# Kernel optimization log

Measured on AMD Instinct MI355X. Metric: run time of the kernel, lower is better.

The kernel has to match this reference:

```python
import jax, jax.numpy as jnp
import numpy as np

N_EDGES = 6000
NUM_IMGS = 5  # 1 reference + 4 source views
H = W = 800
NUM_HALF_V = 10  # hardcoded in sample_points_2d


def setup_inputs() -> dict:
    rng = np.random.default_rng(0)
    # 3D edge endpoints in camera space, in front of the camera
    start = rng.normal(0.0, 0.3, (N_EDGES, 3)).astype(np.float32)
    start[:, 2] += 2.5
    d = rng.normal(size=(N_EDGES, 3))
    d /= np.linalg.norm(d, axis=1, keepdims=True)
    length = rng.uniform(0.3, 0.7, (N_EDGES, 1))
    end = (start + d * length).astype(np.float32)
    # num_horizontal = clamp(norm/0.01, 2, 1000) -- integer, no gradient, so
    # the ragged coordinate template is precomputed here (faithful to torch)
    num_h = np.clip((np.linalg.norm(end - start, axis=-1) / 0.01).astype(np.int64), 2, 1000)
    edge_idx_x = np.repeat(np.arange(N_EDGES), num_h)
    begin = np.concatenate(([0], np.cumsum(num_h)[:-1]))
    dx = (np.arange(num_h.sum()) - begin[edge_idx_x]) / (num_h - 1)[edge_idx_x]
    dy = np.arange(NUM_HALF_V) / (NUM_HALF_V - 1)
    dy = np.concatenate((-dy[::-1], dy))  # [20]
    coords_x = np.repeat(dx, 2 * NUM_HALF_V).astype(np.float32)  # [T]
    coords_y = np.tile(dy, int(num_h.sum())).astype(np.float32)  # [T]
    edge_idx = np.repeat(edge_idx_x, 2 * NUM_HALF_V).astype(np.int64)  # [T]
    num_per_edge = (num_h * NUM_HALF_V * 2).astype(np.int64)  # [N]
    imgs = rng.random((NUM_IMGS, H, W)).astype(np.float32)
    intrinsic = np.array([[0.8, 0.0, 0.5], [0.0, 0.8, 0.5], [0.0, 0.0, 1.0]], dtype=np.float32)
    trans = np.zeros((NUM_IMGS - 1, 3, 4), dtype=np.float32)
    for i in range(NUM_IMGS - 1):
        Rt = np.eye(3, 4, dtype=np.float32)
        Rt[:, 3] = rng.normal(0.0, 0.05, 3)
        trans[i] = intrinsic @ Rt
    return {
        'start_points': jnp.asarray(start),
        'end_points': jnp.asarray(end),
        'imgs': jnp.asarray(imgs),
        'transformations': jnp.asarray(trans),
        'intrinsic': jnp.asarray(intrinsic),
        'coords_x': jnp.asarray(coords_x),
        'coords_y': jnp.asarray(coords_y),
        'edge_idx': jnp.asarray(edge_idx),
        'num_per_edge': jnp.asarray(num_per_edge),
    }


def _bilinear(img, uv):
    # img [H,W], uv [T,2] in [0,1); grid_sample(align_corners=False) convention
    Hh, Ww = img.shape
    x = uv[:, 0] * Ww - 0.5
    y = uv[:, 1] * Hh - 0.5
    x0 = jnp.floor(x)
    y0 = jnp.floor(y)
    wx = x - x0
    wy = y - y0
    x0i = jnp.clip(x0.astype(jnp.int32), 0, Ww - 1)
    x1i = jnp.clip(x0i + 1, 0, Ww - 1)
    y0i = jnp.clip(y0.astype(jnp.int32), 0, Hh - 1)
    y1i = jnp.clip(y0i + 1, 0, Hh - 1)
    v00 = img[y0i, x0i]
    v01 = img[y0i, x1i]
    v10 = img[y1i, x0i]
    v11 = img[y1i, x1i]
    return (v00 * (1 - wx) + v01 * wx) * (1 - wy) + (v10 * (1 - wx) + v11 * wx) * wy


def reference(start_points, end_points, imgs, transformations, intrinsic,
              coords_x, coords_y, edge_idx, num_per_edge):
    num_src = imgs.shape[0] - 1
    img_w = imgs.shape[2]
    n_edges = start_points.shape[0]
    # interleave endpoints: [2N,3]
    points_c = jnp.stack([start_points, end_points], axis=1).reshape(-1, 3)

    def sample_template(ep):
        # ep: [N,2,2] projected 2D edge endpoints -> per-coordinate 2D points [T,2]
        p0 = ep[:, 0]
        cur_dir = ep[:, 1] - ep[:, 0]
        dir3 = jnp.concatenate([cur_dir, jnp.zeros_like(cur_dir[:, :1])], axis=1)
        z = jnp.zeros_like(dir3).at[:, 2].set(1.0)
        c = jnp.cross(dir3, z)[:, :2]
        edge_up = c / (jnp.linalg.norm(c, axis=-1, keepdims=True) + 1e-6) * (10.0 / img_w)
        return (cur_dir[edge_idx] * coords_x[:, None]
                + edge_up[edge_idx] * coords_y[:, None]
                + p0[edge_idx])

    # reference view projection (pinhole, normalized coords)
    proj = (intrinsic @ points_c.T).T
    ep1 = (proj[:, :2] / (proj[:, 2:3] + 1e-6)).reshape(-1, 2, 2)
    p2d1 = sample_template(ep1)  # [T,2]
    vm1 = jnp.all((p2d1 > 0) & (p2d1 < 1), axis=-1)
    p2d1 = jnp.clip(p2d1, 0.0, 0.999999)

    # source view projections
    hom = jnp.concatenate([points_c, jnp.ones_like(points_c[:, :1])], axis=1)  # [2N,4]
    projs = jnp.einsum('sij,nj->sni', transformations, hom)
    ep2 = (projs[..., :2] / (projs[..., 2:3] + 1e-6)).reshape(num_src, -1, 2, 2)
    p2d2 = jax.vmap(sample_template)(ep2)  # [S,T,2]
    vm2 = jnp.all((p2d2 > 0) & (p2d2 < 1), axis=-1)
    p2d2 = jnp.clip(p2d2, 0.0, 0.999999)

    # bilinear image sampling (irregular gather)
    s1 = _bilinear(imgs[0], p2d1)  # [T]
    s2 = jax.vmap(_bilinear)(imgs[1:], p2d2)  # [S,T]

    # loss4: per-edge mean squared photometric difference; black-area detection
    cnt = num_per_edge.astype(jnp.float32)
    seg_sum = lambda v: jax.ops.segment_sum(v, edge_idx, num_segments=n_edges)
    diff2 = (s2 - s1[None, :]) ** 2  # [S,T]
    similarity_loss = jax.vmap(seg_sum)(diff2) / cnt[None, :]  # [S,N]
    black_area = (seg_sum((s1 < 0.01).astype(jnp.float32)) / cnt) > 0.5  # [N]

    # scatter_min of per-point validity -> per-edge mask
    sim_mask_pts = (vm1[None, :] & vm2).astype(jnp.int32)  # [S,T]
    seg_min = lambda m: jax.ops.segment_min(m, edge_idx, num_segments=n_edges)
    similarity_mask = jax.vmap(seg_min)(sim_mask_pts).astype(bool)  # [S,N]

    return similarity_loss, similarity_mask, black_area, p2d1, p2d2
```

## Files before the change

### kernel.cpp

```cpp
#include <hip/hip_runtime.h>
#include <math.h>

#define IMG_W   800
#define IMG_PIX (IMG_W * IMG_W)
#define NEDGE   6000
#define NSRC    4
#define NVIEW   5
#define HDR (2 * NSRC * NEDGE + NEDGE)

typedef float vf4 __attribute__((ext_vector_type(4)));
typedef float vf2 __attribute__((ext_vector_type(2)));

struct __attribute__((packed, aligned(4))) f2u { float a, b; };

__device__ __forceinline__ f2u ld2(const float* __restrict__ p) {
    return *(const f2u*)p;
}
__device__ __forceinline__ void nts2(float* p, float a, float b) {
    vf2 v; v.x = a; v.y = b;
    __builtin_nontemporal_store(v, (vf2*)p);
}
__device__ __forceinline__ void nts4(float* p, float a, float b, float c, float d) {
    vf4 v; v.x = a; v.y = b; v.z = c; v.w = d;
    __builtin_nontemporal_store(v, (vf4*)p);
}

__global__ void edge_params(const float* __restrict__ sp,
                            const float* __restrict__ epnt,
                            const float* __restrict__ K,
                            const float* __restrict__ T,
                            float4* __restrict__ prm) {
    int e = blockIdx.x * blockDim.x + threadIdx.x;
    if (e >= NEDGE) return;
    float sx = sp[3 * e], sy = sp[3 * e + 1], sz = sp[3 * e + 2];
    float ex = epnt[3 * e], ey = epnt[3 * e + 1], ez = epnt[3 * e + 2];
    for (int v = 0; v < NVIEW; ++v) {
        float as, bs, cs, ae, be, ce;
        if (v == 0) {
            as = K[0] * sx + K[1] * sy + K[2] * sz;
            bs = K[3] * sx + K[4] * sy + K[5] * sz;
            cs = K[6] * sx + K[7] * sy + K[8] * sz;
            ae = K[0] * ex + K[1] * ey + K[2] * ez;
            be = K[3] * ex + K[4] * ey + K[5] * ez;
            ce = K[6] * ex + K[7] * ey + K[8] * ez;
        } else {
            const float* t = T + (v - 1) * 12;
            as = t[0] * sx + t[1] * sy + t[2] * sz + t[3];
            bs = t[4] * sx + t[5] * sy + t[6] * sz + t[7];
            cs = t[8] * sx + t[9] * sy + t[10] * sz + t[11];
            ae = t[0] * ex + t[1] * ey + t[2] * ez + t[3];
            be = t[4] * ex + t[5] * ey + t[6] * ez + t[7];
            ce = t[8] * ex + t[9] * ey + t[10] * ez + t[11];
        }
        float u0 = as / (cs + 1e-6f);
        float w0 = bs / (cs + 1e-6f);
        float u1 = ae / (ce + 1e-6f);
        float w1 = be / (ce + 1e-6f);
        float dx = u1 - u0, dy = w1 - w0;
        float cxx = dy, cyy = -dx;
        float nrm = sqrtf(cxx * cxx + cyy * cyy);
        float inv = 1.f / (nrm + 1e-6f) * (10.0f / (float)IMG_W);
        prm[(e * NVIEW + v) * 2 + 0] = make_float4(u0, w0, dx, dy);
        prm[(e * NVIEW + v) * 2 + 1] = make_float4(cxx * inv, cyy * inv, 0.f, 0.f);
    }
}

__global__ void __launch_bounds__(256)
scan_kernel(const int* __restrict__ npe, int* __restrict__ bg) {
    __shared__ int part[256];
    int t = threadIdx.x;
    int base = t * 24;
    int loc[24];
    int s = 0;
#pragma unroll
    for (int i = 0; i < 24; ++i) {
        int idx = base + i;
        int v = (idx < NEDGE) ? npe[idx] : 0;
        loc[i] = s;
        s += v;
    }
    part[t] = s;
    __syncthreads();
    int own = s;
    for (int off = 1; off < 256; off <<= 1) {
        int v = (t >= off) ? part[t - off] : 0;
        __syncthreads();
        part[t] += v;
        __syncthreads();
    }
    int myoff = part[t] - own;
#pragma unroll
    for (int i = 0; i < 24; ++i) {
        int idx = base + i;
        if (idx < NEDGE) bg[idx] = myoff + loc[i];
    }
}

__global__ void __launch_bounds__(256)
points_kernel(const int* __restrict__ npe,
              const int* __restrict__ bg,
              const float* __restrict__ imgs,
              const float4* __restrict__ prm,
              float* __restrict__ out,
              int P) {
    const int e = blockIdx.x;
    const int nsamp = npe[e];
    const int nh = nsamp / 20;
    const int b20 = bg[e];

    __shared__ float DX[1000];
    __shared__ float DY[20];
    __shared__ float rS[4][5];
    __shared__ int   rM[4];

    for (int h = threadIdx.x; h < nh; h += 256)
        DX[h] = (float)((double)h / (double)(nh - 1));
    if (threadIdx.x < 20) {
        int m = threadIdx.x;
        DY[m] = (m < 10) ? -(float)((double)(9 - m) / 9.0)
                         :  (float)((double)(m - 10) / 9.0);
    }

    float4 A[NVIEW], B[NVIEW];
    {
        const float4* pe = prm + (size_t)e * (NVIEW * 2);
#pragma unroll
        for (int v = 0; v < NVIEW; ++v) { A[v] = pe[2 * v]; B[v] = pe[2 * v + 1]; }
    }
    __syncthreads();

    float accs[NSRC] = {0.f, 0.f, 0.f, 0.f};
    float accB = 0.f;
    unsigned maskAcc = 0x1Fu;

    for (int base = 0; base < nsamp; base += 256 * 4) {
        const int t = threadIdx.x;
        bool fullIter = (base + 1024) <= nsamp;
        if (fullIter) {
            int pidx[4];
            pidx[0] = base + 2 * t;
            pidx[1] = pidx[0] + 1;
            pidx[2] = pidx[0] + 512;
            pidx[3] = pidx[2] + 1;

            float px[4 * NVIEW], py[4 * NVIEW];
            unsigned vmb[4];
#pragma unroll
            for (int k = 0; k < 4; ++k) {
                int p = pidx[k];
                int h = p / 20;
                int m = p - h * 20;
                float xk = DX[h];
                float yk = DY[m];
                unsigned mb = 0;
#pragma unroll
                for (int v = 0; v < NVIEW; ++v) {
                    float ux = A[v].z * xk + B[v].x * yk + A[v].x;
                    float uy = A[v].w * xk + B[v].y * yk + A[v].y;
                    if ((ux > 0.f) && (ux < 1.f) && (uy > 0.f) && (uy < 1.f)) mb |= (1u << v);
                    px[k * NVIEW + v] = fminf(fmaxf(ux, 0.f), 0.999999f);
                    py[k * NVIEW + v] = fminf(fmaxf(uy, 0.f), 0.999999f);
                }
                vmb[k] = mb;
                maskAcc &= mb;
            }

            size_t gb = (size_t)(b20 + base);
#pragma unroll
            for (int v = 0; v < NVIEW; ++v) {
                float* bp = (v == 0) ? (out + HDR + 2 * gb)
                                     : (out + HDR + 2 * (size_t)P
                                            + 2 * ((size_t)(v - 1) * P + gb));
                nts4(bp + 4 * t,        px[0 * NVIEW + v], py[0 * NVIEW + v],
                                        px[1 * NVIEW + v], py[1 * NVIEW + v]);
                nts4(bp + 1024 + 4 * t, px[2 * NVIEW + v], py[2 * NVIEW + v],
                                        px[3 * NVIEW + v], py[3 * NVIEW + v]);
            }

            f2u r0[4 * NVIEW], r1[4 * NVIEW];
            unsigned hib[4] = {0, 0, 0, 0};
#pragma unroll
            for (int k = 0; k < 4; ++k) {
#pragma unroll
                for (int v = 0; v < NVIEW; ++v) {
                    int j = k * NVIEW + v;
                    float fx = px[j] * (float)IMG_W - 0.5f;
                    float fy = py[j] * (float)IMG_W - 0.5f;
                    float xf = floorf(fx), yf = floorf(fy);
                    px[j] = fx - xf;
                    py[j] = fy - yf;
                    int x0 = (int)xf;
                    int y0 = (int)yf;
                    int xc = min(max(x0, 0), IMG_W - 2);
                    int y0i = min(max(y0, 0), IMG_W - 1);
                    int y1i = min(y0i + 1, IMG_W - 1);
                    if (x0 >= IMG_W - 1) hib[k] |= (1u << v);
                    const float* im = imgs + v * IMG_PIX;
                    r0[j] = ld2(im + y0i * IMG_W + xc);
                    r1[j] = ld2(im + y1i * IMG_W + xc);
                }
            }
#pragma unroll
            for (int k = 0; k < 4; ++k) {
                float sval[NVIEW];
#pragma unroll
                for (int v = 0; v < NVIEW; ++v) {
                    int j = k * NVIEW + v;
                    bool hi = (hib[k] >> v) & 1u;
                    float v00 = hi ? r0[j].b : r0[j].a;
                    float v01 = r0[j].b;
                    float v10 = hi ? r1[j].b : r1[j].a;
                    float v11 = r1[j].b;
                    float wxv = px[j], wyv = py[j];
                    sval[v] = (v00 * (1.f - wxv) + v01 * wxv) * (1.f - wyv)
                            + (v10 * (1.f - wxv) + v11 * wxv) * wyv;
                }
                float s1 = sval[0];
                accB += (s1 < 0.01f) ? 1.f : 0.f;
#pragma unroll
                for (int s = 0; s < NSRC; ++s) {
                    float d = sval[s + 1] - s1;
                    accs[s] += d * d;
                }
            }
        } else {
            int pidx[4];
            pidx[0] = base + 2 * t;
            pidx[1] = pidx[0] + 1;
            pidx[2] = pidx[0] + 512;
            pidx[3] = pidx[2] + 1;
#pragma unroll
            for (int k = 0; k < 4; ++k) {
                int p = pidx[k];
                if (p >= nsamp) continue;
                int h = p / 20;
                int m = p - h * 20;
                float xk = DX[h];
                float yk = DY[m];
                unsigned mb = 0;
                float lpx[NVIEW], lpy[NVIEW];
#pragma unroll
                for (int v = 0; v < NVIEW; ++v) {
                    float ux = A[v].z * xk + B[v].x * yk + A[v].x;
                    float uy = A[v].w * xk + B[v].y * yk + A[v].y;
                    if ((ux > 0.f) && (ux < 1.f) && (uy > 0.f) && (uy < 1.f)) mb |= (1u << v);
                    lpx[v] = fminf(fmaxf(ux, 0.f), 0.999999f);
                    lpy[v] = fminf(fmaxf(uy, 0.f), 0.999999f);
                }
                maskAcc &= mb;
                size_t g = (size_t)(b20 + p);
                nts2(out + HDR + 2 * g, lpx[0], lpy[0]);
#pragma unroll
                for (int s = 0; s < NSRC; ++s)
                    nts2(out + HDR + 2 * (size_t)P + 2 * ((size_t)s * P + g),
                         lpx[s + 1], lpy[s + 1]);
                float sval[NVIEW];
#pragma unroll
                for (int v = 0; v < NVIEW; ++v) {
                    float fx = lpx[v] * (float)IMG_W - 0.5f;
                    float fy = lpy[v] * (float)IMG_W - 0.5f;
                    float xf = floorf(fx), yf = floorf(fy);
                    float wxv = fx - xf, wyv = fy - yf;
                    int x0 = (int)xf;
                    int y0 = (int)yf;
                    int xc = min(max(x0, 0), IMG_W - 2);
                    int y0i = min(max(y0, 0), IMG_W - 1);
                    int y1i = min(y0i + 1, IMG_W - 1);
                    bool hi = (x0 >= IMG_W - 1);
                    const float* im = imgs + v * IMG_PIX;
                    f2u a = ld2(im + y0i * IMG_W + xc);
                    f2u b = ld2(im + y1i * IMG_W + xc);
                    float v00 = hi ? a.b : a.a;
                    float v01 = a.b;
                    float v10 = hi ? b.b : b.a;
                    float v11 = b.b;
                    sval[v] = (v00 * (1.f - wxv) + v01 * wxv) * (1.f - wyv)
                            + (v10 * (1.f - wxv) + v11 * wxv) * wyv;
                }
                float s1 = sval[0];
                accB += (s1 < 0.01f) ? 1.f : 0.f;
#pragma unroll
                for (int s = 0; s < NSRC; ++s) {
                    float d = sval[s + 1] - s1;
                    accs[s] += d * d;
                }
            }
        }
    }

    int lane = threadIdx.x & 63, wid = threadIdx.x >> 6;
    int mi = (int)maskAcc;
#pragma unroll
    for (int off = 32; off > 0; off >>= 1) {
        accs[0] += __shfl_down(accs[0], off);
        accs[1] += __shfl_down(accs[1], off);
        accs[2] += __shfl_down(accs[2], off);
        accs[3] += __shfl_down(accs[3], off);
        accB    += __shfl_down(accB, off);
        mi      &= __shfl_down(mi, off);
    }
    if (lane == 0) {
        rS[wid][0] = accs[0]; rS[wid][1] = accs[1];
        rS[wid][2] = accs[2]; rS[wid][3] = accs[3];
        rS[wid][4] = accB;
        rM[wid] = mi;
    }
    __syncthreads();
    if (threadIdx.x == 0) {
        float s0 = 0.f, s1 = 0.f, s2 = 0.f, s3 = 0.f, sB = 0.f;
        int m = 0x1F;
#pragma unroll
        for (int w = 0; w < 4; ++w) {
            s0 += rS[w][0]; s1 += rS[w][1]; s2 += rS[w][2]; s3 += rS[w][3];
            sB += rS[w][4];
            m  &= rM[w];
        }
        float cnt = (float)nsamp;
        out[0 * NEDGE + e] = s0 / cnt;
        out[1 * NEDGE + e] = s1 / cnt;
        out[2 * NEDGE + e] = s2 / cnt;
        out[3 * NEDGE + e] = s3 / cnt;
        bool vm1 = m & 1;
#pragma unroll
        for (int s = 0; s < NSRC; ++s)
            out[NSRC * NEDGE + s * NEDGE + e] =
                (vm1 && ((m >> (s + 1)) & 1)) ? 1.f : 0.f;
        out[2 * NSRC * NEDGE + e] = ((sB / cnt) > 0.5f) ? 1.f : 0.f;
    }
}

extern "C" void kernel_launch(void* const* d_in, const int* in_sizes, int n_in,
                              void* d_out, int out_size, void* d_ws, size_t ws_size,
                              hipStream_t stream) {
    const float* start = (const float*)d_in[0];
    const float* endp  = (const float*)d_in[1];
    const float* imgs  = (const float*)d_in[2];
    const float* trans = (const float*)d_in[3];
    const float* K     = (const float*)d_in[4];
    const int*   npe   = (const int*)d_in[8];
    int P = in_sizes[5];

    float4* prm = (float4*)d_ws;
    int*    bg  = (int*)((char*)d_ws + NEDGE * NVIEW * 2 * 16);

    float* out = (float*)d_out;
    edge_params<<<(NEDGE + 255) / 256, 256, 0, stream>>>(start, endp, K, trans, prm);
    scan_kernel<<<1, 256, 0, stream>>>(npe, bg);
    points_kernel<<<NEDGE, 256, 0, stream>>>(npe, bg, imgs, prm, out, P);
}
```

Baseline: 398.3 us.

## Process two points per thread per iteration with uniform edge params and unified tail

Each thread now handles two consecutive samples per loop step instead of four, which shrinks the per-thread register arrays and drops the separate scalar tail path in favour of one guarded path. Per-edge projection parameters are broadcast with readfirstlane so they can sit in scalar registers, and output base pointers are computed once per block. Nontemporal 16-byte stores are used only when the destination is 64-byte aligned; otherwise ordinary stores are issued. The aim is lower VGPR pressure and higher occupancy, at the cost of more loop iterations and fewer gathers in flight per thread.

```diff
diff --git a/kernel.cpp b/kernel.cpp
--- a/kernel.cpp
+++ b/kernel.cpp
@@ -16,13 +16,15 @@
 __device__ __forceinline__ f2u ld2(const float* __restrict__ p) {
     return *(const f2u*)p;
 }
-__device__ __forceinline__ void nts2(float* p, float a, float b) {
-    vf2 v; v.x = a; v.y = b;
-    __builtin_nontemporal_store(v, (vf2*)p);
-}
-__device__ __forceinline__ void nts4(float* p, float a, float b, float c, float d) {
+__device__ __forceinline__ float rfl(float x) {
+    return __uint_as_float((unsigned)__builtin_amdgcn_readfirstlane(
+        (int)__float_as_uint(x)));
+}
+__device__ __forceinline__ void st4(float* p, float a, float b, float c, float d,
+                                    bool nt) {
     vf4 v; v.x = a; v.y = b; v.z = c; v.w = d;
-    __builtin_nontemporal_store(v, (vf4*)p);
+    if (nt) __builtin_nontemporal_store(v, (vf4*)p);
+    else    *(vf4*)p = v;
 }
 
 __global__ void edge_params(const float* __restrict__ sp,
@@ -100,7 +102,7 @@
 points_kernel(const int* __restrict__ npe,
               const int* __restrict__ bg,
               const float* __restrict__ imgs,
-              const float4* __restrict__ prm,
+              const float* __restrict__ prm,
               float* __restrict__ out,
               int P) {
     const int e = blockIdx.x;
@@ -121,11 +123,31 @@
                          :  (float)((double)(m - 10) / 9.0);
     }
 
-    float4 A[NVIEW], B[NVIEW];
+    float Ax[NVIEW], Ay[NVIEW], Az[NVIEW], Aw[NVIEW], Bx[NVIEW], By[NVIEW];
     {
-        const float4* pe = prm + (size_t)e * (NVIEW * 2);
-#pragma unroll
-        for (int v = 0; v < NVIEW; ++v) { A[v] = pe[2 * v]; B[v] = pe[2 * v + 1]; }
+        const float* pe = prm + (size_t)e * (NVIEW * 8);
+#pragma unroll
+        for (int v = 0; v < NVIEW; ++v) {
+            Ax[v] = rfl(pe[8 * v + 0]);
+            Ay[v] = rfl(pe[8 * v + 1]);
+            Az[v] = rfl(pe[8 * v + 2]);
+            Aw[v] = rfl(pe[8 * v + 3]);
+            Bx[v] = rfl(pe[8 * v + 4]);
+            By[v] = rfl(pe[8 * v + 5]);
+        }
+    }
+
+    float* vbase[NVIEW];
+    bool   val64[NVIEW];
+    {
+        size_t gb = (size_t)b20;
+        vbase[0] = out + HDR + 2 * gb;
+#pragma unroll
+        for (int s = 0; s < NSRC; ++s)
+            vbase[s + 1] = out + HDR + 2 * (size_t)P + 2 * ((size_t)s * P + gb);
+#pragma unroll
+        for (int v = 0; v < NVIEW; ++v)
+            val64[v] = ((((size_t)vbase[v]) & 63) == 0);
     }
     __syncthreads();
 
@@ -133,21 +155,16 @@
     float accB = 0.f;
     unsigned maskAcc = 0x1Fu;
 
-    for (int base = 0; base < nsamp; base += 256 * 4) {
-        const int t = threadIdx.x;
-        bool fullIter = (base + 1024) <= nsamp;
-        if (fullIter) {
-            int pidx[4];
-            pidx[0] = base + 2 * t;
-            pidx[1] = pidx[0] + 1;
-            pidx[2] = pidx[0] + 512;
-            pidx[3] = pidx[2] + 1;
-
-            float px[4 * NVIEW], py[4 * NVIEW];
-            unsigned vmb[4];
-#pragma unroll
-            for (int k = 0; k < 4; ++k) {
-                int p = pidx[k];
+    const int t = threadIdx.x;
+    for (int base = 0; base < nsamp; base += 512) {
+        int p0 = base + 2 * t;
+        bool valid = (p0 < nsamp);
+
+        float px[2 * NVIEW], py[2 * NVIEW];
+        if (valid) {
+#pragma unroll
+            for (int k = 0; k < 2; ++k) {
+                int p = p0 + k;
                 int h = p / 20;
                 int m = p - h * 20;
                 float xk = DX[h];
@@ -155,32 +172,27 @@
                 unsigned mb = 0;
 #pragma unroll
                 for (int v = 0; v < NVIEW; ++v) {
-                    float ux = A[v].z * xk + B[v].x * yk + A[v].x;
-                    float uy = A[v].w * xk + B[v].y * yk + A[v].y;
-                    if ((ux > 0.f) && (ux < 1.f) && (uy > 0.f) && (uy < 1.f)) mb |= (1u << v);
+                    float ux = Az[v] * xk + Bx[v] * yk + Ax[v];
+                    float uy = Aw[v] * xk + By[v] * yk + Ay[v];
+                    if ((ux > 0.f) && (ux < 1.f) && (uy > 0.f) && (uy < 1.f))
+                        mb |= (1u << v);
                     px[k * NVIEW + v] = fminf(fmaxf(ux, 0.f), 0.999999f);
                     py[k * NVIEW + v] = fminf(fmaxf(uy, 0.f), 0.999999f);
                 }
-                vmb[k] = mb;
                 maskAcc &= mb;
             }
 
-            size_t gb = (size_t)(b20 + base);
 #pragma unroll
             for (int v = 0; v < NVIEW; ++v) {
-                float* bp = (v == 0) ? (out + HDR + 2 * gb)
-                                     : (out + HDR + 2 * (size_t)P
-                                            + 2 * ((size_t)(v - 1) * P + gb));
-                nts4(bp + 4 * t,        px[0 * NVIEW + v], py[0 * NVIEW + v],
-                                        px[1 * NVIEW + v], py[1 * NVIEW + v]);
-                nts4(bp + 1024 + 4 * t, px[2 * NVIEW + v], py[2 * NVIEW + v],
-                                        px[3 * NVIEW + v], py[3 * NVIEW + v]);
+                st4(vbase[v] + 2 * base + 4 * t,
+                    px[0 * NVIEW + v], py[0 * NVIEW + v],
+                    px[1 * NVIEW + v], py[1 * NVIEW + v], val64[v]);
             }
 
-            f2u r0[4 * NVIEW], r1[4 * NVIEW];
-            unsigned hib[4] = {0, 0, 0, 0};
-#pragma unroll
-            for (int k = 0; k < 4; ++k) {
+            f2u r0[2 * NVIEW], r1[2 * NVIEW];
+            unsigned hib = 0;
+#pragma unroll
+            for (int k = 0; k < 2; ++k) {
 #pragma unroll
                 for (int v = 0; v < NVIEW; ++v) {
                     int j = k * NVIEW + v;
@@ -194,86 +206,24 @@
                     int xc = min(max(x0, 0), IMG_W - 2);
                     int y0i = min(max(y0, 0), IMG_W - 1);
                     int y1i = min(y0i + 1, IMG_W - 1);
-                    if (x0 >= IMG_W - 1) hib[k] |= (1u << v);
+                    if (x0 >= IMG_W - 1) hib |= (1u << j);
                     const float* im = imgs + v * IMG_PIX;
                     r0[j] = ld2(im + y0i * IMG_W + xc);
                     r1[j] = ld2(im + y1i * IMG_W + xc);
                 }
             }
 #pragma unroll
-            for (int k = 0; k < 4; ++k) {
+            for (int k = 0; k < 2; ++k) {
                 float sval[NVIEW];
 #pragma unroll
                 for (int v = 0; v < NVIEW; ++v) {
                     int j = k * NVIEW + v;
-                    bool hi = (hib[k] >> v) & 1u;
+                    bool hi = (hib >> j) & 1u;
                     float v00 = hi ? r0[j].b : r0[j].a;
                     float v01 = r0[j].b;
                     float v10 = hi ? r1[j].b : r1[j].a;
                     float v11 = r1[j].b;
                     float wxv = px[j], wyv = py[j];
-                    sval[v] = (v00 * (1.f - wxv) + v01 * wxv) * (1.f - wyv)
-                            + (v10 * (1.f - wxv) + v11 * wxv) * wyv;
-                }
-                float s1 = sval[0];
-                accB += (s1 < 0.01f) ? 1.f : 0.f;
-#pragma unroll
-                for (int s = 0; s < NSRC; ++s) {
-                    float d = sval[s + 1] - s1;
-                    accs[s] += d * d;
-                }
-            }
-        } else {
-            int pidx[4];
-            pidx[0] = base + 2 * t;
-            pidx[1] = pidx[0] + 1;
-            pidx[2] = pidx[0] + 512;
-            pidx[3] = pidx[2] + 1;
-#pragma unroll
-            for (int k = 0; k < 4; ++k) {
-                int p = pidx[k];
-                if (p >= nsamp) continue;
-                int h = p / 20;
-                int m = p - h * 20;
-                float xk = DX[h];
-                float yk = DY[m];
-                unsigned mb = 0;
-                float lpx[NVIEW], lpy[NVIEW];
-#pragma unroll
-                for (int v = 0; v < NVIEW; ++v) {
-                    float ux = A[v].z * xk + B[v].x * yk + A[v].x;
-                    float uy = A[v].w * xk + B[v].y * yk + A[v].y;
-                    if ((ux > 0.f) && (ux < 1.f) && (uy > 0.f) && (uy < 1.f)) mb |= (1u << v);
-                    lpx[v] = fminf(fmaxf(ux, 0.f), 0.999999f);
-                    lpy[v] = fminf(fmaxf(uy, 0.f), 0.999999f);
-                }
-                maskAcc &= mb;
-                size_t g = (size_t)(b20 + p);
-                nts2(out + HDR + 2 * g, lpx[0], lpy[0]);
-#pragma unroll
-                for (int s = 0; s < NSRC; ++s)
-                    nts2(out + HDR + 2 * (size_t)P + 2 * ((size_t)s * P + g),
-                         lpx[s + 1], lpy[s + 1]);
-                float sval[NVIEW];
-#pragma unroll
-                for (int v = 0; v < NVIEW; ++v) {
-                    float fx = lpx[v] * (float)IMG_W - 0.5f;
-                    float fy = lpy[v] * (float)IMG_W - 0.5f;
-                    float xf = floorf(fx), yf = floorf(fy);
-                    float wxv = fx - xf, wyv = fy - yf;
-                    int x0 = (int)xf;
-                    int y0 = (int)yf;
-                    int xc = min(max(x0, 0), IMG_W - 2);
-                    int y0i = min(max(y0, 0), IMG_W - 1);
-                    int y1i = min(y0i + 1, IMG_W - 1);
-                    bool hi = (x0 >= IMG_W - 1);
-                    const float* im = imgs + v * IMG_PIX;
-                    f2u a = ld2(im + y0i * IMG_W + xc);
-                    f2u b = ld2(im + y1i * IMG_W + xc);
-                    float v00 = hi ? a.b : a.a;
-                    float v01 = a.b;
-                    float v10 = hi ? b.b : b.a;
-                    float v11 = b.b;
                     sval[v] = (v00 * (1.f - wxv) + v01 * wxv) * (1.f - wyv)
                             + (v10 * (1.f - wxv) + v11 * wxv) * wyv;
                 }
@@ -346,5 +296,5 @@
     float* out = (float*)d_out;
     edge_params<<<(NEDGE + 255) / 256, 256, 0, stream>>>(start, endp, K, trans, prm);
     scan_kernel<<<1, 256, 0, stream>>>(npe, bg);
-    points_kernel<<<NEDGE, 256, 0, stream>>>(npe, bg, imgs, prm, out, P);
-}
+    points_kernel<<<NEDGE, 256, 0, stream>>>(npe, bg, imgs, (const float*)prm, out, P);
+}
```

New measurement: 385.0 us. 1.03x faster.
